# Kernel tuning notes

Measured on AMD Instinct MI355X. Metric: run time of the kernel, lower is better.

## Reference

```python
import jax, jax.numpy as jnp
import numpy as np

B, N, C, H, P = 8, 4096, 256, 4, 64  # batch, tokens, hidden, heads, proj_size


def setup_inputs() -> dict:
    key = jax.random.key(0)
    ks = jax.random.split(key, 6)
    sc = 0.02
    x = jax.random.normal(ks[0], (B, N, C), jnp.float32)
    bank = jax.random.normal(ks[1], (B, N, C), jnp.float32)  # unused by forward, kept for fidelity
    W_qkvv = jax.random.normal(ks[2], (4 * C, C), jnp.float32) * sc  # Linear(C, 4C), no bias
    W_E = jax.random.normal(ks[3], (P, N), jnp.float32) * sc          # E = F shared Linear(N, P)
    b_E = jnp.zeros((P,), jnp.float32)
    temperature = jnp.ones((H, 1, 1), jnp.float32)
    temperature2 = jnp.ones((H, 1, 1), jnp.float32)
    W_out1 = jax.random.normal(ks[4], (C // 2, C), jnp.float32) * sc  # out_proj (spatial branch)
    b_out1 = jnp.zeros((C // 2,), jnp.float32)
    W_out2 = jax.random.normal(ks[5], (C // 2, C), jnp.float32) * sc  # out_proj2 (channel branch)
    b_out2 = jnp.zeros((C // 2,), jnp.float32)
    prelu_a = jnp.array(0.25, jnp.float32)  # nn.PReLU() default: single shared slope
    return {"x": x, "bank": bank, "W_qkvv": W_qkvv, "W_E": W_E, "b_E": b_E,
            "temperature": temperature, "temperature2": temperature2,
            "W_out1": W_out1, "b_out1": b_out1, "W_out2": W_out2, "b_out2": b_out2,
            "prelu_a": prelu_a}


def _l2norm(t):
    # torch F.normalize(dim=-1): x / max(||x||_2, eps)
    return t / jnp.maximum(jnp.linalg.norm(t, axis=-1, keepdims=True), 1e-12)


def reference(x, bank, W_qkvv, W_E, b_E, temperature, temperature2,
              W_out1, b_out1, W_out2, b_out2, prelu_a):
    Bb, Nn, Cc = x.shape
    Hh = temperature.shape[0]
    d = Cc // Hh
    # qkvv projection -> [4, B, H, N, d], then transpose token/feature axes -> [B, H, d, N]
    qkvv = (x @ W_qkvv.T).reshape(Bb, Nn, 4, Hh, d).transpose(2, 0, 3, 1, 4)
    q, k, v_ca, v_sa = (qkvv[0].transpose(0, 1, 3, 2), qkvv[1].transpose(0, 1, 3, 2),
                        qkvv[2].transpose(0, 1, 3, 2), qkvv[3].transpose(0, 1, 3, 2))
    # shared linear E=F projects the token axis N -> P (applied to UNnormalized k, v_sa)
    k_proj = jnp.einsum('bhdn,pn->bhdp', k, W_E) + b_E      # [B,H,d,P]
    v_sa_proj = jnp.einsum('bhdn,pn->bhdp', v_sa, W_E) + b_E  # [B,H,d,P]
    qn = _l2norm(q)
    kn = _l2norm(k)
    # channel attention: [B,H,d,d]
    attn_ca = jax.nn.softmax(jnp.einsum('bhdn,bhen->bhde', qn, kn) * temperature, axis=-1)
    x_ca = jnp.einsum('bhde,bhen->bhdn', attn_ca, v_ca).transpose(0, 3, 1, 2).reshape(Bb, Nn, Cc)
    # spatial attention (projected): [B,H,N,P]
    attn_sa = jax.nn.softmax(jnp.einsum('bhdn,bhdp->bhnp', qn, k_proj) * temperature2, axis=-1)
    x_sa = jnp.einsum('bhnp,bhdp->bhnd', attn_sa, v_sa_proj).transpose(0, 2, 1, 3).reshape(Bb, Nn, Cc)
    x_sa = x_sa @ W_out1.T + b_out1
    x_ca = x_ca @ W_out2.T + b_out2
    out = jnp.concatenate([x_sa, x_ca], axis=-1)
    return jnp.where(out >= 0, out, prelu_a * out)  # PReLU
```

## Files before the change

### kernel.cpp

```cpp
#include <hip/hip_runtime.h>
#include <cstdint>
#include <cstddef>

constexpr int B_ = 8, N_ = 4096, C_ = 256, H_ = 4, D_ = 64, P_ = 64;
constexpr int OC_ = 4 * C_;
constexpr int M_  = B_ * N_;
constexpr int NC_SPLIT = 16;
constexpr int PAIR_ELEMS = 32 * 3 * 4096;

#define DEV_INLINE __device__ __forceinline__

typedef unsigned short ushort_t;
typedef __attribute__((ext_vector_type(8))) short short8;
typedef __attribute__((ext_vector_type(4))) short short4v;
typedef __attribute__((ext_vector_type(4))) float floatx4;

DEV_INLINE short f2bf(float f) {
  unsigned int u = __builtin_bit_cast(unsigned int, f);
  u += 0x7FFFu + ((u >> 16) & 1u);
  return (short)(u >> 16);
}

constexpr size_t X4_ = (size_t)M_ * C_ / 4;
constexpr size_t WQ4_ = (size_t)OC_ * C_ / 4;
constexpr size_t W14_ = (size_t)128 * C_ / 4;
constexpr size_t TOT4_ = X4_ + WQ4_ + 2 * W14_;

__global__ __launch_bounds__(256) void k_cast(const float* __restrict__ x,
                                              const float* __restrict__ Wq,
                                              const float* __restrict__ W1,
                                              const float* __restrict__ W2,
                                              ushort_t* __restrict__ xb,
                                              ushort_t* __restrict__ wqb,
                                              ushort_t* __restrict__ w1b,
                                              ushort_t* __restrict__ w2b) {
  const size_t stride = (size_t)gridDim.x * 256;
  for (size_t i = blockIdx.x * 256 + threadIdx.x; i < TOT4_; i += stride) {
    const float* src;
    ushort_t* dst;
    size_t o;
    if (i < X4_) { src = x; dst = xb; o = i; }
    else if (i < X4_ + WQ4_) { src = Wq; dst = wqb; o = i - X4_; }
    else if (i < X4_ + WQ4_ + W14_) { src = W1; dst = w1b; o = i - X4_ - WQ4_; }
    else { src = W2; dst = w2b; o = i - X4_ - WQ4_ - W14_; }
    float4 v = ((const float4*)src)[o];
    short4v s = {f2bf(v.x), f2bf(v.y), f2bf(v.z), f2bf(v.w)};
    *(short4v*)&dst[o * 4] = s;
  }
}

__global__ __launch_bounds__(256) void k_qkvv_mfma(const ushort_t* __restrict__ xb,
                                                   const ushort_t* __restrict__ wqb,
                                                   ushort_t* __restrict__ outb,
                                                   float* __restrict__ ssq) {
  __shared__ __align__(16) short As[128 * 72];
  __shared__ __align__(16) short Bs[128 * 72];
  const int bm = blockIdx.x * 128;
  const int bo = blockIdx.y * 128;
  const int t = threadIdx.x;
  const int oc = t & 7;
  const int rr = t >> 3;
  const int lane = t & 63, wave = t >> 6;
  const int m16 = lane & 15, quad = lane >> 4;
  const int wm = (wave >> 1) << 6, wn = (wave & 1) << 6;
  floatx4 acc[4][4];
#pragma unroll
  for (int i = 0; i < 4; ++i)
#pragma unroll
    for (int j = 0; j < 4; ++j) acc[i][j] = (floatx4)(0.f);
#pragma unroll 1
  for (int k0 = 0; k0 < 256; k0 += 64) {
    short8 a8[4], b8[4];
#pragma unroll
    for (int j = 0; j < 4; ++j) {
      const int r = rr + 32 * j;
      a8[j] = *(const short8*)&xb[(size_t)(bm + r) * 256 + k0 + 8 * oc];
      b8[j] = *(const short8*)&wqb[(size_t)(bo + r) * 256 + k0 + 8 * oc];
    }
    __syncthreads();
#pragma unroll
    for (int j = 0; j < 4; ++j) {
      const int r = rr + 32 * j;
      *(short8*)&As[r * 72 + 8 * oc] = a8[j];
      *(short8*)&Bs[r * 72 + 8 * oc] = b8[j];
    }
    __syncthreads();
#pragma unroll
    for (int ks = 0; ks < 2; ++ks) {
      short8 af[4], bf[4];
#pragma unroll
      for (int i = 0; i < 4; ++i)
        af[i] = *(const short8*)&As[(wm + i * 16 + m16) * 72 + ks * 32 + quad * 8];
// ... 2 lines not shown
        bf[j] = *(const short8*)&Bs[(wn + j * 16 + m16) * 72 + ks * 32 + quad * 8];
#pragma unroll
      for (int i = 0; i < 4; ++i)
#pragma unroll
        for (int j = 0; j < 4; ++j)
          acc[i][j] = __builtin_amdgcn_mfma_f32_16x16x32_bf16(af[i], bf[j], acc[i][j], 0, 0, 0);
    }
  }
#pragma unroll
  for (int i = 0; i < 4; ++i)
#pragma unroll
    for (int r = 0; r < 4; ++r) {
      const int gr = bm + wm + i * 16 + quad * 4 + r;
#pragma unroll
      for (int j = 0; j < 4; ++j)
        outb[(size_t)gr * OC_ + bo + wn + j * 16 + m16] = (ushort_t)f2bf(acc[i][j][r]);
    }
  if (bo < 512) {
    const int b = bm >> 12;
    float sj[4];
#pragma unroll
    for (int j = 0; j < 4; ++j) {
      float s = 0.f;
#pragma unroll
      for (int i = 0; i < 4; ++i)
#pragma unroll
        for (int r = 0; r < 4; ++r) s += acc[i][j][r] * acc[i][j][r];
      s += __shfl_xor(s, 16);
      s += __shfl_xor(s, 32);
      sj[j] = s;
    }
    if (lane < 16) {
#pragma unroll
      for (int j = 0; j < 4; ++j)
        atomicAdd(&ssq[b * 512 + bo + wn + 16 * j + m16], sj[j]);
    }
  }
}

__global__ __launch_bounds__(256) void k_out_mfma(const ushort_t* __restrict__ xsa,
                                                  const ushort_t* __restrict__ xca,
                                                  const ushort_t* __restrict__ w1b,
                                                  const float* __restrict__ b1,
                                                  const ushort_t* __restrict__ w2b,
                                                  const float* __restrict__ b2,
                                                  const float* __restrict__ pa,
                                                  float* __restrict__ out) {
  __shared__ __align__(16) short As[128 * 72];
  __shared__ __align__(16) short Bs[128 * 72];
  const int bm = blockIdx.x * 128;
  const int half = blockIdx.y;
  const ushort_t* A = half ? xca : xsa;
// ... 49 lines not shown
  for (int j = 0; j < 4; ++j) bj[j] = bias[wn + j * 16 + m16];
#pragma unroll
  for (int i = 0; i < 4; ++i)
#pragma unroll
    for (int r = 0; r < 4; ++r) {
      const int gr = bm + wm + i * 16 + quad * 4 + r;
#pragma unroll
      for (int j = 0; j < 4; ++j) {
        float v = acc[i][j][r] + bj[j];
        v = v >= 0.f ? v : slope * v;
        out[(size_t)gr * C_ + half * 128 + wn + j * 16 + m16] = v;
      }
    }
}

__global__ void k_norms_final(const float* __restrict__ ssq, float* __restrict__ rn) {
  const int i = blockIdx.x * 256 + threadIdx.x;
  rn[i] = 1.f / fmaxf(sqrtf(ssq[i]), 1e-12f);
}

__global__ __launch_bounds__(256) void k_pair_mfma(const ushort_t* __restrict__ qkvv,
                                                   const float* __restrict__ WE,
                                                   float* __restrict__ pp) {
  __shared__ __align__(16) short Qt[64 * 64];
  __shared__ __align__(16) short Kt[64 * 64];
  __shared__ __align__(16) short Vt[64 * 64];
  __shared__ __align__(16) short Wt[64 * 64];
  const int bh = blockIdx.x;
  const int nc = blockIdx.y;
  const int b = bh >> 2, h = bh & 3;
  const int t = threadIdx.x;
  const int lane = t & 63, wave = t >> 6;
  const int m16 = lane & 15, quad = lane >> 4;
  const int c0 = (t & 15) << 2;
  const int tp = t >> 4;
  floatx4 acc0[4], acc1[4], acc2[4];
#pragma unroll
  for (int j = 0; j < 4; ++j) {
    acc0[j] = (floatx4)(0.f); acc1[j] = (floatx4)(0.f); acc2[j] = (floatx4)(0.f);
  }
  const ushort_t* qb = qkvv + (size_t)b * N_ * OC_;
#pragma unroll 1
  for (int chunk = 0; chunk < 4; ++chunk) {
    const int n0 = nc * 256 + chunk * 64;
    __syncthreads();
#pragma unroll
    for (int j = 0; j < 2; ++j) {
      const int tok0 = 32 * j + 2 * tp;
      const size_t r0 = (size_t)(n0 + tok0) * OC_ + h * 64 + c0;
#pragma unroll
      for (int tt = 0; tt < 3; ++tt) {
        const int off = (tt == 0) ? 0 : (tt == 1 ? 256 : 768);
        short* T = (tt == 0) ? Qt : (tt == 1 ? Kt : Vt);
        short4v a = *(const short4v*)&qb[r0 + off];
        short4v c = *(const short4v*)&qb[r0 + OC_ + off];
#pragma unroll
        for (int i = 0; i < 4; ++i) {
          const int r = c0 + i;
          const int col = tok0 ^ (8 * (r >> 3));
          unsigned int w = (unsigned int)(ushort_t)a[i] |
                           ((unsigned int)(ushort_t)c[i] << 16);
          *(unsigned int*)&T[r * 64 + col] = w;
        }
      }
    }
#pragma unroll
    for (int j2 = 0; j2 < 4; ++j2) {
      const int p = tp + 16 * j2;
      float4 wv = *(const float4*)&WE[(size_t)p * N_ + n0 + c0];
      short4v s = {f2bf(wv.x), f2bf(wv.y), f2bf(wv.z), f2bf(wv.w)};
      *(short4v*)&Wt[p * 64 + (c0 ^ (8 * (p >> 3)))] = s;
    }
    __syncthreads();
#pragma unroll
    for (int ks = 0; ks < 2; ++ks) {
      const int boct = ks * 32 + quad * 8;
      const int rA = 16 * wave + m16;
      const int swA = boct ^ (8 * (rA >> 3));
      short8 af0 = *(const short8*)&Qt[rA * 64 + swA];
      short8 afK = *(const short8*)&Kt[rA * 64 + swA];
      short8 afV = *(const short8*)&Vt[rA * 64 + swA];
      short8 bfK[4], bfW[4];
#pragma unroll
      for (int j = 0; j < 4; ++j) {
        const int rB = 16 * j + m16;
        const int swB = boct ^ (8 * (rB >> 3));
        bfK[j] = *(const short8*)&Kt[rB * 64 + swB];
        bfW[j] = *(const short8*)&Wt[rB * 64 + swB];
      }
#pragma unroll
      for (int j = 0; j < 4; ++j) {
        acc0[j] = __builtin_amdgcn_mfma_f32_16x16x32_bf16(af0, bfK[j], acc0[j], 0, 0, 0);
        acc1[j] = __builtin_amdgcn_mfma_f32_16x16x32_bf16(afK, bfW[j], acc1[j], 0, 0, 0);
        acc2[j] = __builtin_amdgcn_mfma_f32_16x16x32_bf16(afV, bfW[j], acc2[j], 0, 0, 0);
      }
    }
  }
  float* pb = pp + ((size_t)nc * 32 + bh) * (3 * 4096);
#pragma unroll
  for (int j = 0; j < 4; ++j)
#pragma unroll
    for (int r = 0; r < 4; ++r) {
      const int d = 16 * wave + quad * 4 + r;
      const int cc = 16 * j + m16;
      pb[0 * 4096 + d * 64 + cc] = acc0[j][r];
      pb[1 * 4096 + cc * 64 + d] = acc1[j][r];
      pb[2 * 4096 + d * 64 + cc] = acc2[j][r];
    }
}

__global__ __launch_bounds__(256) void k_pair_reduce(const float* __restrict__ pp,
                                                     const float* __restrict__ bE,
                                                     const float* __restrict__ rn,
                                                     const float* __restrict__ t2,
                                                     float* __restrict__ Sqk,
                                                     ushort_t* __restrict__ ksb,
                                                     ushort_t* __restrict__ vsb) {
  const int e = blockIdx.x * 256 + threadIdx.x;
  float s = 0.f;
#pragma unroll
  for (int nc = 0; nc < NC_SPLIT; ++nc) s += pp[(size_t)nc * PAIR_ELEMS + e];
  const int bh = e / 12288;
  const int rem = e - bh * 12288;
  const int op = rem >> 12;
  const int idx = rem & 4095;
  const int b = bh >> 2, h = bh & 3;
  if (op == 0) {
    Sqk[(size_t)bh * 4096 + idx] = s;
  } else if (op == 1) {
    const int p = idx >> 6, d = idx & 63;
    ksb[(size_t)bh * 4096 + idx] =
        (ushort_t)f2bf((s + bE[p]) * rn[b * 512 + h * 64 + d] * t2[h]);
  } else {
    const int p = idx & 63;
    vsb[(size_t)bh * 4096 + idx] = (ushort_t)f2bf(s + bE[p]);
  }
}

__global__ __launch_bounds__(256) void k_ca_softmax(const float* __restrict__ Sqk,
                                                    const float* __restrict__ rn,
                                                    const float* __restrict__ temp,
                                                    ushort_t* __restrict__ ab) {
  const int w = threadIdx.x >> 6;
  const int lane = threadIdx.x & 63;
  const int row = blockIdx.x * 4 + w;
  const int b = row >> 8;
  const int rem = row & 255;
  const int h = rem >> 6;
  const float rq = rn[b * 512 + rem];
  const float rk = rn[b * 512 + 256 + h * 64 + lane];
  float l = Sqk[(size_t)row * 64 + lane] * rq * rk * temp[h];
  float m = l;
#pragma unroll
  for (int o = 32; o; o >>= 1) m = fmaxf(m, __shfl_xor(m, o));
  const float e = __expf(l - m);
  float s = e;
#pragma unroll
  for (int o = 32; o; o >>= 1) s += __shfl_xor(s, o);
  ab[(size_t)row * 64 + lane] = (ushort_t)f2bf(e / s);
}

__global__ __launch_bounds__(256) void k_ca_mfma(const ushort_t* __restrict__ qkvv,
                                                 const ushort_t* __restrict__ ab,
                                                 ushort_t* __restrict__ x_ca) {
  const int bh = blockIdx.x;
  const int b = bh >> 2, h = bh & 3;
  const int n0 = blockIdx.y * 128;
  const int lane = threadIdx.x & 63, wave = threadIdx.x >> 6;
  const int m16 = lane & 15, quad = lane >> 4;
  const ushort_t* abb = ab + (size_t)bh * 4096;
  short8 bf[2][4];
#pragma unroll
  for (int ks = 0; ks < 2; ++ks)
#pragma unroll
    for (int j = 0; j < 4; ++j)
      bf[ks][j] = *(const short8*)&abb[(16 * j + m16) * 64 + ks * 32 + quad * 8];
#pragma unroll
  for (int mm = 0; mm < 2; ++mm) {
    const int tokbase = n0 + 64 * mm + 16 * wave;
    const ushort_t* vrow =
        qkvv + (size_t)(b * N_ + tokbase + m16) * OC_ + 512 + h * 64 + quad * 8;
    short8 af0 = *(const short8*)&vrow[0];
    short8 af1 = *(const short8*)&vrow[32];
    floatx4 o[4];
#pragma unroll
    for (int j = 0; j < 4; ++j) o[j] = (floatx4)(0.f);
#pragma unroll
    for (int j = 0; j < 4; ++j) {
      o[j] = __builtin_amdgcn_mfma_f32_16x16x32_bf16(af0, bf[0][j], o[j], 0, 0, 0);
      o[j] = __builtin_amdgcn_mfma_f32_16x16x32_bf16(af1, bf[1][j], o[j], 0, 0, 0);
    }
#pragma unroll
    for (int j = 0; j < 4; ++j)
#pragma unroll
      for (int r = 0; r < 4; ++r)
        x_ca[(size_t)(b * N_ + tokbase + quad * 4 + r) * C_ + h * 64 + 16 * j + m16] =
            (ushort_t)f2bf(o[j][r]);
  }
}

__global__ __launch_bounds__(256) void k_sa_mfma(const ushort_t* __restrict__ qkvv,
                                                 const ushort_t* __restrict__ ksb,
                                                 const ushort_t* __restrict__ vsb,
                                                 ushort_t* __restrict__ x_sa) {
  __shared__ float Pl[64][68];
  const int bh = blockIdx.x;
  const int b = bh >> 2, h = bh & 3;
  const int n0 = blockIdx.y * 64;
  const int lane = threadIdx.x & 63, wave = threadIdx.x >> 6;
  const int m16 = lane & 15, quad = lane >> 4;
  const ushort_t* qrow =
      qkvv + (size_t)(b * N_ + n0 + 16 * wave + m16) * OC_ + h * 64 + quad * 8;
  short8 qf0 = *(const short8*)&qrow[0];
  short8 qf1 = *(const short8*)&qrow[32];
  const ushort_t* kb = ksb + (size_t)bh * 4096;
  const ushort_t* vb = vsb + (size_t)bh * 4096;
  short8 kf[2][4], vf[2][4];
#pragma unroll
  for (int ks = 0; ks < 2; ++ks)
#pragma unroll
    for (int j = 0; j < 4; ++j) {
      kf[ks][j] = *(const short8*)&kb[(16 * j + m16) * 64 + ks * 32 + quad * 8];
      vf[ks][j] = *(const short8*)&vb[(16 * j + m16) * 64 + ks * 32 + quad * 8];
    }
  floatx4 s[4];
#pragma unroll
  for (int j = 0; j < 4; ++j) s[j] = (floatx4)(0.f);
#pragma unroll
  for (int j = 0; j < 4; ++j) {
    s[j] = __builtin_amdgcn_mfma_f32_16x16x32_bf16(qf0, kf[0][j], s[j], 0, 0, 0);
    s[j] = __builtin_amdgcn_mfma_f32_16x16x32_bf16(qf1, kf[1][j], s[j], 0, 0, 0);
  }
  float p[4][4];
#pragma unroll
  for (int r = 0; r < 4; ++r) {
    float mr = fmaxf(fmaxf(s[0][r], s[1][r]), fmaxf(s[2][r], s[3][r]));
    mr = fmaxf(mr, __shfl_xor(mr, 1));
    mr = fmaxf(mr, __shfl_xor(mr, 2));
    mr = fmaxf(mr, __shfl_xor(mr, 4));
    mr = fmaxf(mr, __shfl_xor(mr, 8));
    float sr = 0.f;
#pragma unroll
    for (int j = 0; j < 4; ++j) {
      const float e = __expf(s[j][r] - mr);
      p[j][r] = e;
      sr += e;
    }
    sr += __shfl_xor(sr, 1);
    sr += __shfl_xor(sr, 2);
    sr += __shfl_xor(sr, 4);
    sr += __shfl_xor(sr, 8);
    const float inv = 1.f / sr;
#pragma unroll
    for (int j = 0; j < 4; ++j) p[j][r] *= inv;
  }
#pragma unroll
  for (int j = 0; j < 4; ++j)
#pragma unroll
    for (int r = 0; r < 4; ++r)
      Pl[16 * wave + quad * 4 + r][16 * j + m16] = p[j][r];
  __syncthreads();
  short8 pf[2];
#pragma unroll
  for (int ks = 0; ks < 2; ++ks) {
    float4 x0 = *(const float4*)&Pl[16 * wave + m16][ks * 32 + quad * 8];
    float4 x1 = *(const float4*)&Pl[16 * wave + m16][ks * 32 + quad * 8 + 4];
    short8 v;
    v[0] = f2bf(x0.x); v[1] = f2bf(x0.y); v[2] = f2bf(x0.z); v[3] = f2bf(x0.w);
    v[4] = f2bf(x1.x); v[5] = f2bf(x1.y); v[6] = f2bf(x1.z); v[7] = f2bf(x1.w);
    pf[ks] = v;
  }
  floatx4 o[4];
#pragma unroll
  for (int j = 0; j < 4; ++j) o[j] = (floatx4)(0.f);
#pragma unroll
  for (int j = 0; j < 4; ++j) {
    o[j] = __builtin_amdgcn_mfma_f32_16x16x32_bf16(pf[0], vf[0][j], o[j], 0, 0, 0);
    o[j] = __builtin_amdgcn_mfma_f32_16x16x32_bf16(pf[1], vf[1][j], o[j], 0, 0, 0);
  }
#pragma unroll
  for (int j = 0; j < 4; ++j)
#pragma unroll
    for (int r = 0; r < 4; ++r)
      x_sa[(size_t)(b * N_ + n0 + 16 * wave + quad * 4 + r) * C_ + h * 64 + 16 * j + m16] =
          (ushort_t)f2bf(o[j][r]);
}

extern "C" void kernel_launch(void* const* d_in, const int* in_sizes, int n_in,
                              void* d_out, int out_size, void* d_ws, size_t ws_size,
                              hipStream_t stream) {
  (void)in_sizes; (void)n_in; (void)out_size; (void)ws_size;
  const float* x  = (const float*)d_in[0];
  const float* Wq = (const float*)d_in[2];
  const float* WE = (const float*)d_in[3];
  const float* bE = (const float*)d_in[4];
  const float* t1 = (const float*)d_in[5];
  const float* t2 = (const float*)d_in[6];
  const float* W1 = (const float*)d_in[7];
  const float* b1 = (const float*)d_in[8];
  const float* W2 = (const float*)d_in[9];
  const float* b2 = (const float*)d_in[10];
  const float* pa = (const float*)d_in[11];
  float* out = (float*)d_out;

  float* ws = (float*)d_ws;
  size_t off = 0;
  float* Sqk  = ws + off; off += (size_t)B_ * H_ * D_ * D_;
  float* ssq  = ws + off; off += (size_t)B_ * 512;
  float* rn   = ws + off; off += (size_t)B_ * 512;
  float* pp   = ws + off; off += (size_t)NC_SPLIT * PAIR_ELEMS;
  ushort_t* qkvv = (ushort_t*)(ws + off); off += (size_t)M_ * OC_ / 2;
  ushort_t* xsa  = (ushort_t*)(ws + off); off += (size_t)M_ * C_ / 2;
  ushort_t* xca  = (ushort_t*)(ws + off); off += (size_t)M_ * C_ / 2;
  ushort_t* ksb  = (ushort_t*)(ws + off); off += 32 * 4096 / 2;
  ushort_t* vsb  = (ushort_t*)(ws + off); off += 32 * 4096 / 2;
  ushort_t* ab   = (ushort_t*)(ws + off); off += 32 * 4096 / 2;
  ushort_t* xb   = (ushort_t*)(ws + off); off += (size_t)M_ * C_ / 2;
  ushort_t* wqb  = (ushort_t*)(ws + off); off += (size_t)OC_ * C_ / 2;
  ushort_t* w1b  = (ushort_t*)(ws + off); off += (size_t)128 * C_ / 2;
  ushort_t* w2b  = (ushort_t*)(ws + off); off += (size_t)128 * C_ / 2;

  hipMemsetAsync(ssq, 0, 4096 * sizeof(float), stream);

  k_cast<<<2048, 256, 0, stream>>>(x, Wq, W1, W2, xb, wqb, w1b, w2b);
  k_qkvv_mfma<<<dim3(M_ / 128, OC_ / 128), 256, 0, stream>>>(xb, wqb, qkvv, ssq);
  k_norms_final<<<16, 256, 0, stream>>>(ssq, rn);
  k_pair_mfma<<<dim3(32, NC_SPLIT), 256, 0, stream>>>(qkvv, WE, pp);
  k_pair_reduce<<<PAIR_ELEMS / 256, 256, 0, stream>>>(pp, bE, rn, t2, Sqk, ksb, vsb);
  k_ca_softmax<<<512, 256, 0, stream>>>(Sqk, rn, t1, ab);
  k_ca_mfma<<<dim3(32, 32), 256, 0, stream>>>(qkvv, ab, xca);
  k_sa_mfma<<<dim3(32, 64), 256, 0, stream>>>(qkvv, ksb, vsb, xsa);
  k_out_mfma<<<dim3(M_ / 128, 2), 256, 0, stream>>>(xsa, xca, w1b, b1, w2b, b2, pa, out);
}
```

Measured before the change: 227.2 us.

## Derive k and v_sa statistics from input Gram matrix instead of materializing them

Replaces the full qkvv projection with a q/v_ca-only projection. K-side quantities (q·k channel Gram, k norms, k and v_sa token projections through W_E) are now computed from an input Gram matrix X^T X and X^T W_E^T per batch, followed by small GEMMs with the weight matrix. This removes writing and rereading half of the projected activations and drops the separate pair-reduction pass. In exchange it adds several small kernels, an atomic-accumulated fp32 Gram buffer, and extra bf16 rounding of the Gram terms that may cost accuracy.

```diff
diff --git a/kernel.cpp b/kernel.cpp
--- a/kernel.cpp
+++ b/kernel.cpp
@@ -5,8 +5,8 @@
 constexpr int B_ = 8, N_ = 4096, C_ = 256, H_ = 4, D_ = 64, P_ = 64;
 constexpr int OC_ = 4 * C_;
 constexpr int M_  = B_ * N_;
-constexpr int NC_SPLIT = 16;
-constexpr int PAIR_ELEMS = 32 * 3 * 4096;
+constexpr int GX_ROWS = 320;
+constexpr int KSPLIT_G = 8;
 
 #define DEV_INLINE __device__ __forceinline__
 
@@ -20,20 +20,26 @@
   u += 0x7FFFu + ((u >> 16) & 1u);
   return (short)(u >> 16);
 }
-
-constexpr size_t X4_ = (size_t)M_ * C_ / 4;
+DEV_INLINE float bf2f(ushort_t u) {
+  return __builtin_bit_cast(float, (unsigned int)u << 16);
+}
+
+constexpr size_t X4_  = (size_t)M_ * C_ / 4;
 constexpr size_t WQ4_ = (size_t)OC_ * C_ / 4;
 constexpr size_t W14_ = (size_t)128 * C_ / 4;
-constexpr size_t TOT4_ = X4_ + WQ4_ + 2 * W14_;
+constexpr size_t WE4_ = (size_t)P_ * N_ / 4;
+constexpr size_t TOT4_ = X4_ + WQ4_ + 2 * W14_ + WE4_;
 
 __global__ __launch_bounds__(256) void k_cast(const float* __restrict__ x,
                                               const float* __restrict__ Wq,
                                               const float* __restrict__ W1,
                                               const float* __restrict__ W2,
+                                              const float* __restrict__ WE,
                                               ushort_t* __restrict__ xb,
                                               ushort_t* __restrict__ wqb,
                                               ushort_t* __restrict__ w1b,
-                                              ushort_t* __restrict__ w2b) {
+                                              ushort_t* __restrict__ w2b,
+                                              ushort_t* __restrict__ web) {
   const size_t stride = (size_t)gridDim.x * 256;
   for (size_t i = blockIdx.x * 256 + threadIdx.x; i < TOT4_; i += stride) {
     const float* src;
@@ -42,21 +48,137 @@
     if (i < X4_) { src = x; dst = xb; o = i; }
     else if (i < X4_ + WQ4_) { src = Wq; dst = wqb; o = i - X4_; }
     else if (i < X4_ + WQ4_ + W14_) { src = W1; dst = w1b; o = i - X4_ - WQ4_; }
-    else { src = W2; dst = w2b; o = i - X4_ - WQ4_ - W14_; }
+    else if (i < X4_ + WQ4_ + 2 * W14_) { src = W2; dst = w2b; o = i - X4_ - WQ4_ - W14_; }
+    else { src = WE; dst = web; o = i - X4_ - WQ4_ - 2 * W14_; }
     float4 v = ((const float4*)src)[o];
     short4v s = {f2bf(v.x), f2bf(v.y), f2bf(v.z), f2bf(v.w)};
     *(short4v*)&dst[o * 4] = s;
   }
 }
 
-__global__ __launch_bounds__(256) void k_qkvv_mfma(const ushort_t* __restrict__ xb,
-                                                   const ushort_t* __restrict__ wqb,
-                                                   ushort_t* __restrict__ outb,
-                                                   float* __restrict__ ssq) {
+__global__ __launch_bounds__(256) void k_gram(const ushort_t* __restrict__ xb,
+                                              const ushort_t* __restrict__ web,
+                                              float* __restrict__ Gx) {
+  __shared__ __align__(16) short As[128 * 64];
+  __shared__ __align__(16) short Bs[128 * 64];
+  const int job = blockIdx.x;
+  const int ablk = job >> 1;
+  const int bblk = job & 1;
+  const int b = blockIdx.y >> 3;
+  const int ksp = blockIdx.y & 7;
+  const int t = threadIdx.x;
+  const int lane = t & 63, wave = t >> 6;
+  const int m16 = lane & 15, quad = lane >> 4;
+  const int wm = (wave >> 1) << 6, wn = (wave & 1) << 6;
+  floatx4 acc[4][4];
+#pragma unroll
+  for (int i = 0; i < 4; ++i)
+#pragma unroll
+    for (int j = 0; j < 4; ++j) acc[i][j] = (floatx4)(0.f);
+  if (ablk == 2) {
+#pragma unroll
+    for (int i = 0; i < 8; ++i)
+      *(unsigned int*)&As[64 * 64 + (i * 256 + t) * 2] = 0u;
+  }
+  const int c0 = (t & 31) * 4;
+  const int tp = t >> 5;
+#pragma unroll 1
+  for (int it = 0; it < N_ / KSPLIT_G / 64; ++it) {
+    const int n0 = ksp * (N_ / KSPLIT_G) + it * 64;
+    __syncthreads();
+#pragma unroll
+    for (int q = 0; q < 4; ++q) {
+      const int tok = q * 16 + 2 * tp;
+      const size_t r0 = (size_t)(b * N_ + n0 + tok) * C_ + bblk * 128 + c0;
+      short4v aa = *(const short4v*)&xb[r0];
+      short4v cc = *(const short4v*)&xb[r0 + C_];
+#pragma unroll
+      for (int i = 0; i < 4; ++i) {
+        const int r = c0 + i;
+        const int col = tok ^ (8 * ((r >> 3) & 7));
+        unsigned int w = (unsigned int)(ushort_t)aa[i] |
+                         ((unsigned int)(ushort_t)cc[i] << 16);
+        *(unsigned int*)&Bs[r * 64 + col] = w;
+      }
+    }
+    if (ablk < 2) {
+#pragma unroll
+      for (int q = 0; q < 4; ++q) {
+        const int tok = q * 16 + 2 * tp;
+        const size_t r0 = (size_t)(b * N_ + n0 + tok) * C_ + ablk * 128 + c0;
+        short4v aa = *(const short4v*)&xb[r0];
+        short4v cc = *(const short4v*)&xb[r0 + C_];
+#pragma unroll
+        for (int i = 0; i < 4; ++i) {
+          const int r = c0 + i;
+          const int col = tok ^ (8 * ((r >> 3) & 7));
+          unsigned int w = (unsigned int)(ushort_t)aa[i] |
+                           ((unsigned int)(ushort_t)cc[i] << 16);
+          *(unsigned int*)&As[r * 64 + col] = w;
+        }
+      }
+    } else {
+      const int oc8 = (t & 7) * 8;
+      const int p0 = t >> 3;
+#pragma unroll
+      for (int q = 0; q < 2; ++q) {
+        const int p = p0 + 32 * q;
+        short8 v = *(const short8*)&web[(size_t)p * N_ + n0 + oc8];
+        *(short8*)&As[p * 64 + (oc8 ^ (8 * ((p >> 3) & 7)))] = v;
+      }
+    }
+    __syncthreads();
+#pragma unroll
+    for (int ks = 0; ks < 2; ++ks) {
+      const int boct = ks * 32 + quad * 8;
+      short8 af[4], bf[4];
+#pragma unroll
+      for (int i = 0; i < 4; ++i) {
+        const int rA = wm + i * 16 + m16;
+        af[i] = *(const short8*)&As[rA * 64 + (boct ^ (8 * ((rA >> 3) & 7)))];
+      }
+#pragma unroll
+      for (int j = 0; j < 4; ++j) {
+        const int rB = wn + j * 16 + m16;
+        bf[j] = *(const short8*)&Bs[rB * 64 + (boct ^ (8 * ((rB >> 3) & 7)))];
+      }
+#pragma unroll
+      for (int i = 0; i < 4; ++i)
+#pragma unroll
+        for (int j = 0; j < 4; ++j)
+          acc[i][j] = __builtin_amdgcn_mfma_f32_16x16x32_bf16(af[i], bf[j], acc[i][j], 0, 0, 0);
+    }
+  }
+#pragma unroll
+  for (int i = 0; i < 4; ++i)
+#pragma unroll
+    for (int r = 0; r < 4; ++r) {
+      const int rib = wm + i * 16 + quad * 4 + r;
+      if (ablk == 2 && rib >= 64) continue;
+      const size_t rowoff =
+          ((size_t)b * GX_ROWS + ablk * 128 + rib) * 256 + bblk * 128 + wn;
+#pragma unroll
+      for (int j = 0; j < 4; ++j)
+        atomicAdd(&Gx[rowoff + 16 * j + m16], acc[i][j][r]);
+    }
+}
+
+__global__ __launch_bounds__(256) void k_gcast(const float* __restrict__ Gx,
+                                               ushort_t* __restrict__ Gxb) {
+  const int i = blockIdx.x * 256 + threadIdx.x;
+  float4 v = ((const float4*)Gx)[i];
+  short4v s = {f2bf(v.x), f2bf(v.y), f2bf(v.z), f2bf(v.w)};
+  *(short4v*)&Gxb[i * 4] = s;
+}
+
+__global__ __launch_bounds__(256) void k_qv_mfma(const ushort_t* __restrict__ xb,
+                                                 const ushort_t* __restrict__ wqb,
+                                                 ushort_t* __restrict__ qv) {
   __shared__ __align__(16) short As[128 * 72];
   __shared__ __align__(16) short Bs[128 * 72];
   const int bm = blockIdx.x * 128;
   const int bo = blockIdx.y * 128;
+  const int wrow_base = bo < 256 ? bo : bo + 256;
   const int t = threadIdx.x;
   const int oc = t & 7;
   const int rr = t >> 3;
@@ -75,7 +197,7 @@
     for (int j = 0; j < 4; ++j) {
       const int r = rr + 32 * j;
       a8[j] = *(const short8*)&xb[(size_t)(bm + r) * 256 + k0 + 8 * oc];
-      b8[j] = *(const short8*)&wqb[(size_t)(bo + r) * 256 + k0 + 8 * oc];
+      b8[j] = *(const short8*)&wqb[(size_t)(wrow_base + r) * 256 + k0 + 8 * oc];
     }
     __syncthreads();
 #pragma unroll
@@ -108,28 +230,317 @@
       const int gr = bm + wm + i * 16 + quad * 4 + r;
 #pragma unroll
       for (int j = 0; j < 4; ++j)
-        outb[(size_t)gr * OC_ + bo + wn + j * 16 + m16] = (ushort_t)f2bf(acc[i][j][r]);
-    }
-  if (bo < 512) {
-    const int b = bm >> 12;
-    float sj[4];
-#pragma unroll
-    for (int j = 0; j < 4; ++j) {
-      float s = 0.f;
+        qv[(size_t)gr * 512 + bo + wn + j * 16 + m16] = (ushort_t)f2bf(acc[i][j][r]);
+    }
+}
+
+__global__ __launch_bounds__(256) void k_t2gemm(const ushort_t* __restrict__ wqb,
+                                                const ushort_t* __restrict__ Gxb,
+                                                ushort_t* __restrict__ T2b) {
+  __shared__ __align__(16) short As[128 * 72];
+  __shared__ __align__(16) short Bs[128 * 72];
+  const int bm = blockIdx.x * 128;
+  const int b  = blockIdx.y >> 1;
+  const int jb = blockIdx.y & 1;
+  const int t = threadIdx.x;
+  const int oc = t & 7;
+  const int rr = t >> 3;
+  const int lane = t & 63, wave = t >> 6;
+  const int m16 = lane & 15, quad = lane >> 4;
+  const int wm = (wave >> 1) << 6, wn = (wave & 1) << 6;
+  const ushort_t* Bsrc = Gxb + ((size_t)b * GX_ROWS + jb * 128) * 256;
+  floatx4 acc[4][4];
+#pragma unroll
+  for (int i = 0; i < 4; ++i)
+#pragma unroll
+    for (int j = 0; j < 4; ++j) acc[i][j] = (floatx4)(0.f);
+#pragma unroll 1
+  for (int k0 = 0; k0 < 256; k0 += 64) {
+    short8 a8[4], b8[4];
+#pragma unroll
+    for (int j = 0; j < 4; ++j) {
+      const int r = rr + 32 * j;
+      a8[j] = *(const short8*)&wqb[(size_t)(bm + r) * 256 + k0 + 8 * oc];
+      b8[j] = *(const short8*)&Bsrc[(size_t)r * 256 + k0 + 8 * oc];
+    }
+    __syncthreads();
+#pragma unroll
+    for (int j = 0; j < 4; ++j) {
+      const int r = rr + 32 * j;
+      *(short8*)&As[r * 72 + 8 * oc] = a8[j];
+      *(short8*)&Bs[r * 72 + 8 * oc] = b8[j];
+    }
+    __syncthreads();
+#pragma unroll
+    for (int ks = 0; ks < 2; ++ks) {
+      short8 af[4], bf[4];
 #pragma unroll
       for (int i = 0; i < 4; ++i)
-#pragma unroll
-        for (int r = 0; r < 4; ++r) s += acc[i][j][r] * acc[i][j][r];
-      s += __shfl_xor(s, 16);
-      s += __shfl_xor(s, 32);
-      sj[j] = s;
-    }
-    if (lane < 16) {
+        af[i] = *(const short8*)&As[(wm + i * 16 + m16) * 72 + ks * 32 + quad * 8];
 #pragma unroll
       for (int j = 0; j < 4; ++j)
-        atomicAdd(&ssq[b * 512 + bo + wn + 16 * j + m16], sj[j]);
-    }
-  }
+        bf[j] = *(const short8*)&Bs[(wn + j * 16 + m16) * 72 + ks * 32 + quad * 8];
+#pragma unroll
+      for (int i = 0; i < 4; ++i)
+#pragma unroll
+        for (int j = 0; j < 4; ++j)
+          acc[i][j] = __builtin_amdgcn_mfma_f32_16x16x32_bf16(af[i], bf[j], acc[i][j], 0, 0, 0);
+    }
+  }
+#pragma unroll
+  for (int i = 0; i < 4; ++i)
+#pragma unroll
+    for (int r = 0; r < 4; ++r) {
+      const int gr = bm + wm + i * 16 + quad * 4 + r;
+#pragma unroll
+      for (int j = 0; j < 4; ++j)
+        T2b[((size_t)b * 512 + gr) * 256 + jb * 128 + wn + j * 16 + m16] =
+            (ushort_t)f2bf(acc[i][j][r]);
+    }
+}
+
+__global__ __launch_bounds__(256) void k_rn(const ushort_t* __restrict__ wqb,
+                                            const ushort_t* __restrict__ T2b,
+                                            float* __restrict__ rn) {
+  const int row_g = blockIdx.x * 4 + (threadIdx.x >> 6);
+  const int lane = threadIdx.x & 63;
+  const int b = row_g >> 9, row = row_g & 511;
+  const short4v w  = *(const short4v*)&wqb[(size_t)row * 256 + lane * 4];
+  const short4v tv = *(const short4v*)&T2b[((size_t)b * 512 + row) * 256 + lane * 4];
+  float s = 0.f;
+#pragma unroll
+  for (int i = 0; i < 4; ++i) s += bf2f((ushort_t)w[i]) * bf2f((ushort_t)tv[i]);
+#pragma unroll
+  for (int o = 32; o; o >>= 1) s += __shfl_xor(s, o);
+  if (lane == 0) rn[row_g] = 1.f / fmaxf(sqrtf(s), 1e-12f);
+}
+
+__global__ __launch_bounds__(64) void k_small(const ushort_t* __restrict__ wqb,
+                                              const ushort_t* __restrict__ T2b,
+                                              const ushort_t* __restrict__ Gxb,
+                                              const float* __restrict__ bE,
+                                              const float* __restrict__ rn,
+                                              const float* __restrict__ t2,
+                                              float* __restrict__ Sqk,
+                                              ushort_t* __restrict__ ksb,
+                                              ushort_t* __restrict__ vsb) {
+  const int bh = blockIdx.x;
+  const int job = blockIdx.y;
+  const int b = bh >> 2, h = bh & 3;
+  const int lane = threadIdx.x & 63;
+  const int m16 = lane & 15, quad = lane >> 4;
+  const int Abase = (job == 0 ? 0 : (job == 1 ? 256 : 768)) + h * 64;
+  const ushort_t* Bp = (job == 0)
+      ? T2b + ((size_t)b * 512 + 256 + h * 64) * 256
+      : Gxb + ((size_t)b * GX_ROWS + 256) * 256;
+  floatx4 acc[4][4];
+#pragma unroll
+  for (int i = 0; i < 4; ++i)
+#pragma unroll
+    for (int j = 0; j < 4; ++j) acc[i][j] = (floatx4)(0.f);
+#pragma unroll
+  for (int ks = 0; ks < 8; ++ks) {
+    const int boct = ks * 32 + quad * 8;
+    short8 af[4], bf[4];
+#pragma unroll
+    for (int i = 0; i < 4; ++i)
+      af[i] = *(const short8*)&wqb[(size_t)(Abase + 16 * i + m16) * 256 + boct];
+#pragma unroll
+    for (int j = 0; j < 4; ++j)
+      bf[j] = *(const short8*)&Bp[(size_t)(16 * j + m16) * 256 + boct];
+#pragma unroll
+    for (int i = 0; i < 4; ++i)
+#pragma unroll
+      for (int j = 0; j < 4; ++j)
+        acc[i][j] = __builtin_amdgcn_mfma_f32_16x16x32_bf16(af[i], bf[j], acc[i][j], 0, 0, 0);
+  }
+  if (job == 0) {
+#pragma unroll
+    for (int i = 0; i < 4; ++i)
+#pragma unroll
+      for (int r = 0; r < 4; ++r) {
+        const int d = 16 * i + quad * 4 + r;
+#pragma unroll
+        for (int j = 0; j < 4; ++j)
+          Sqk[(size_t)bh * 4096 + d * 64 + 16 * j + m16] = acc[i][j][r];
+      }
+  } else if (job == 1) {
+    const float tt = t2[h];
+#pragma unroll
+    for (int i = 0; i < 4; ++i)
+#pragma unroll
+      for (int r = 0; r < 4; ++r) {
+        const int d = 16 * i + quad * 4 + r;
+        const float rq = rn[b * 512 + h * 64 + d];
+#pragma unroll
+        for (int j = 0; j < 4; ++j) {
+          const int p = 16 * j + m16;
+          ksb[(size_t)bh * 4096 + p * 64 + d] =
+              (ushort_t)f2bf((acc[i][j][r] + bE[p]) * rq * tt);
+        }
+      }
+  } else {
+#pragma unroll
+    for (int i = 0; i < 4; ++i)
+#pragma unroll
+      for (int r = 0; r < 4; ++r) {
+        const int d = 16 * i + quad * 4 + r;
+#pragma unroll
+        for (int j = 0; j < 4; ++j) {
+          const int p = 16 * j + m16;
+          vsb[(size_t)bh * 4096 + d * 64 + p] = (ushort_t)f2bf(acc[i][j][r] + bE[p]);
+        }
+      }
+  }
+}
+
+__global__ __launch_bounds__(256) void k_ca_softmax(const float* __restrict__ Sqk,
+                                                    const float* __restrict__ rn,
+                                                    const float* __restrict__ temp,
+                                                    ushort_t* __restrict__ ab) {
+  const int w = threadIdx.x >> 6;
+  const int lane = threadIdx.x & 63;
+  const int row = blockIdx.x * 4 + w;
+  const int b = row >> 8;
+  const int rem = row & 255;
+  const int h = rem >> 6;
+  const float rq = rn[b * 512 + rem];
+  const float rk = rn[b * 512 + 256 + h * 64 + lane];
+  float l = Sqk[(size_t)row * 64 + lane] * rq * rk * temp[h];
+  float m = l;
+#pragma unroll
+  for (int o = 32; o; o >>= 1) m = fmaxf(m, __shfl_xor(m, o));
+  const float e = __expf(l - m);
+  float s = e;
+#pragma unroll
+  for (int o = 32; o; o >>= 1) s += __shfl_xor(s, o);
+  ab[(size_t)row * 64 + lane] = (ushort_t)f2bf(e / s);
+}
+
+__global__ __launch_bounds__(256) void k_ca_mfma(const ushort_t* __restrict__ qv,
+                                                 const ushort_t* __restrict__ ab,
+                                                 ushort_t* __restrict__ x_ca) {
+  const int bh = blockIdx.x;
+  const int b = bh >> 2, h = bh & 3;
+  const int n0 = blockIdx.y * 128;
+  const int lane = threadIdx.x & 63, wave = threadIdx.x >> 6;
+  const int m16 = lane & 15, quad = lane >> 4;
+  const ushort_t* abb = ab + (size_t)bh * 4096;
+  short8 bf[2][4];
+#pragma unroll
+  for (int ks = 0; ks < 2; ++ks)
+#pragma unroll
+    for (int j = 0; j < 4; ++j)
+      bf[ks][j] = *(const short8*)&abb[(16 * j + m16) * 64 + ks * 32 + quad * 8];
+#pragma unroll
+  for (int mm = 0; mm < 2; ++mm) {
+    const int tokbase = n0 + 64 * mm + 16 * wave;
+    const ushort_t* vrow =
+        qv + (size_t)(b * N_ + tokbase + m16) * 512 + 256 + h * 64 + quad * 8;
+    short8 af0 = *(const short8*)&vrow[0];
+    short8 af1 = *(const short8*)&vrow[32];
+    floatx4 o[4];
+#pragma unroll
+    for (int j = 0; j < 4; ++j) o[j] = (floatx4)(0.f);
+#pragma unroll
+    for (int j = 0; j < 4; ++j) {
+      o[j] = __builtin_amdgcn_mfma_f32_16x16x32_bf16(af0, bf[0][j], o[j], 0, 0, 0);
+      o[j] = __builtin_amdgcn_mfma_f32_16x16x32_bf16(af1, bf[1][j], o[j], 0, 0, 0);
+    }
+#pragma unroll
+    for (int j = 0; j < 4; ++j)
+#pragma unroll
+      for (int r = 0; r < 4; ++r)
+        x_ca[(size_t)(b * N_ + tokbase + quad * 4 + r) * C_ + h * 64 + 16 * j + m16] =
+            (ushort_t)f2bf(o[j][r]);
+  }
+}
+
+__global__ __launch_bounds__(256) void k_sa_mfma(const ushort_t* __restrict__ qv,
+                                                 const ushort_t* __restrict__ ksb,
+                                                 const ushort_t* __restrict__ vsb,
+                                                 ushort_t* __restrict__ x_sa) {
+  __shared__ float Pl[64][68];
+  const int bh = blockIdx.x;
+  const int b = bh >> 2, h = bh & 3;
+  const int n0 = blockIdx.y * 64;
+  const int lane = threadIdx.x & 63, wave = threadIdx.x >> 6;
+  const int m16 = lane & 15, quad = lane >> 4;
+  const ushort_t* qrow =
+      qv + (size_t)(b * N_ + n0 + 16 * wave + m16) * 512 + h * 64 + quad * 8;
+  short8 qf0 = *(const short8*)&qrow[0];
+  short8 qf1 = *(const short8*)&qrow[32];
+  const ushort_t* kb = ksb + (size_t)bh * 4096;
+  const ushort_t* vb = vsb + (size_t)bh * 4096;
+  short8 kf[2][4], vf[2][4];
+#pragma unroll
+  for (int ks = 0; ks < 2; ++ks)
+#pragma unroll
+    for (int j = 0; j < 4; ++j) {
+      kf[ks][j] = *(const short8*)&kb[(16 * j + m16) * 64 + ks * 32 + quad * 8];
+      vf[ks][j] = *(const short8*)&vb[(16 * j + m16) * 64 + ks * 32 + quad * 8];
+    }
+  floatx4 s[4];
+#pragma unroll
+  for (int j = 0; j < 4; ++j) s[j] = (floatx4)(0.f);
+#pragma unroll
+  for (int j = 0; j < 4; ++j) {
+    s[j] = __builtin_amdgcn_mfma_f32_16x16x32_bf16(qf0, kf[0][j], s[j], 0, 0, 0);
+    s[j] = __builtin_amdgcn_mfma_f32_16x16x32_bf16(qf1, kf[1][j], s[j], 0, 0, 0);
+  }
+  float p[4][4];
+#pragma unroll
+  for (int r = 0; r < 4; ++r) {
+    float mr = fmaxf(fmaxf(s[0][r], s[1][r]), fmaxf(s[2][r], s[3][r]));
+    mr = fmaxf(mr, __shfl_xor(mr, 1));
+    mr = fmaxf(mr, __shfl_xor(mr, 2));
+    mr = fmaxf(mr, __shfl_xor(mr, 4));
+    mr = fmaxf(mr, __shfl_xor(mr, 8));
+    float sr = 0.f;
+#pragma unroll
+    for (int j = 0; j < 4; ++j) {
+      const float e = __expf(s[j][r] - mr);
+      p[j][r] = e;
+      sr += e;
+    }
+    sr += __shfl_xor(sr, 1);
+    sr += __shfl_xor(sr, 2);
+    sr += __shfl_xor(sr, 4);
+    sr += __shfl_xor(sr, 8);
+    const float inv = 1.f / sr;
+#pragma unroll
+    for (int j = 0; j < 4; ++j) p[j][r] *= inv;
+  }
+#pragma unroll
+  for (int j = 0; j < 4; ++j)
+#pragma unroll
+    for (int r = 0; r < 4; ++r)
+      Pl[16 * wave + quad * 4 + r][16 * j + m16] = p[j][r];
+  __syncthreads();
+  short8 pf[2];
+#pragma unroll
+  for (int ks = 0; ks < 2; ++ks) {
+    float4 x0 = *(const float4*)&Pl[16 * wave + m16][ks * 32 + quad * 8];
+    float4 x1 = *(const float4*)&Pl[16 * wave + m16][ks * 32 + quad * 8 + 4];
+    short8 v;
+    v[0] = f2bf(x0.x); v[1] = f2bf(x0.y); v[2] = f2bf(x0.z); v[3] = f2bf(x0.w);
+    v[4] = f2bf(x1.x); v[5] = f2bf(x1.y); v[6] = f2bf(x1.z); v[7] = f2bf(x1.w);
+    pf[ks] = v;
+  }
+  floatx4 o[4];
+#pragma unroll
+  for (int j = 0; j < 4; ++j) o[j] = (floatx4)(0.f);
+#pragma unroll
+  for (int j = 0; j < 4; ++j) {
+    o[j] = __builtin_amdgcn_mfma_f32_16x16x32_bf16(pf[0], vf[0][j], o[j], 0, 0, 0);
+    o[j] = __builtin_amdgcn_mfma_f32_16x16x32_bf16(pf[1], vf[1][j], o[j], 0, 0, 0);
+  }
+#pragma unroll
+  for (int j = 0; j < 4; ++j)
+#pragma unroll
+    for (int r = 0; r < 4; ++r)
+      x_sa[(size_t)(b * N_ + n0 + 16 * wave + quad * 4 + r) * C_ + h * 64 + 16 * j + m16] =
+          (ushort_t)f2bf(o[j][r]);
 }
 
 __global__ __launch_bounds__(256) void k_out_mfma(const ushort_t* __restrict__ xsa,
@@ -209,278 +620,6 @@
     }
 }
 
-__global__ void k_norms_final(const float* __restrict__ ssq, float* __restrict__ rn) {
-  const int i = blockIdx.x * 256 + threadIdx.x;
-  rn[i] = 1.f / fmaxf(sqrtf(ssq[i]), 1e-12f);
-}
-
-__global__ __launch_bounds__(256) void k_pair_mfma(const ushort_t* __restrict__ qkvv,
-                                                   const float* __restrict__ WE,
-                                                   float* __restrict__ pp) {
-  __shared__ __align__(16) short Qt[64 * 64];
-  __shared__ __align__(16) short Kt[64 * 64];
-  __shared__ __align__(16) short Vt[64 * 64];
-  __shared__ __align__(16) short Wt[64 * 64];
-  const int bh = blockIdx.x;
-  const int nc = blockIdx.y;
-  const int b = bh >> 2, h = bh & 3;
-  const int t = threadIdx.x;
-  const int lane = t & 63, wave = t >> 6;
-  const int m16 = lane & 15, quad = lane >> 4;
-  const int c0 = (t & 15) << 2;
-  const int tp = t >> 4;
-  floatx4 acc0[4], acc1[4], acc2[4];
-#pragma unroll
-  for (int j = 0; j < 4; ++j) {
-    acc0[j] = (floatx4)(0.f); acc1[j] = (floatx4)(0.f); acc2[j] = (floatx4)(0.f);
-  }
-  const ushort_t* qb = qkvv + (size_t)b * N_ * OC_;
-#pragma unroll 1
-  for (int chunk = 0; chunk < 4; ++chunk) {
-    const int n0 = nc * 256 + chunk * 64;
-    __syncthreads();
-#pragma unroll
-    for (int j = 0; j < 2; ++j) {
-      const int tok0 = 32 * j + 2 * tp;
-      const size_t r0 = (size_t)(n0 + tok0) * OC_ + h * 64 + c0;
-#pragma unroll
-      for (int tt = 0; tt < 3; ++tt) {
-        const int off = (tt == 0) ? 0 : (tt == 1 ? 256 : 768);
-        short* T = (tt == 0) ? Qt : (tt == 1 ? Kt : Vt);
-        short4v a = *(const short4v*)&qb[r0 + off];
-        short4v c = *(const short4v*)&qb[r0 + OC_ + off];
-#pragma unroll
-        for (int i = 0; i < 4; ++i) {
-          const int r = c0 + i;
-          const int col = tok0 ^ (8 * (r >> 3));
-          unsigned int w = (unsigned int)(ushort_t)a[i] |
-                           ((unsigned int)(ushort_t)c[i] << 16);
-          *(unsigned int*)&T[r * 64 + col] = w;
-        }
-      }
-    }
-#pragma unroll
-    for (int j2 = 0; j2 < 4; ++j2) {
-      const int p = tp + 16 * j2;
-      float4 wv = *(const float4*)&WE[(size_t)p * N_ + n0 + c0];
-      short4v s = {f2bf(wv.x), f2bf(wv.y), f2bf(wv.z), f2bf(wv.w)};
-      *(short4v*)&Wt[p * 64 + (c0 ^ (8 * (p >> 3)))] = s;
-    }
-    __syncthreads();
-#pragma unroll
-    for (int ks = 0; ks < 2; ++ks) {
-      const int boct = ks * 32 + quad * 8;
-      const int rA = 16 * wave + m16;
-      const int swA = boct ^ (8 * (rA >> 3));
-      short8 af0 = *(const short8*)&Qt[rA * 64 + swA];
-      short8 afK = *(const short8*)&Kt[rA * 64 + swA];
-      short8 afV = *(const short8*)&Vt[rA * 64 + swA];
-      short8 bfK[4], bfW[4];
-#pragma unroll
-      for (int j = 0; j < 4; ++j) {
-        const int rB = 16 * j + m16;
-        const int swB = boct ^ (8 * (rB >> 3));
-        bfK[j] = *(const short8*)&Kt[rB * 64 + swB];
-        bfW[j] = *(const short8*)&Wt[rB * 64 + swB];
-      }
-#pragma unroll
-      for (int j = 0; j < 4; ++j) {
-        acc0[j] = __builtin_amdgcn_mfma_f32_16x16x32_bf16(af0, bfK[j], acc0[j], 0, 0, 0);
-        acc1[j] = __builtin_amdgcn_mfma_f32_16x16x32_bf16(afK, bfW[j], acc1[j], 0, 0, 0);
-        acc2[j] = __builtin_amdgcn_mfma_f32_16x16x32_bf16(afV, bfW[j], acc2[j], 0, 0, 0);
-      }
-    }
-  }
-  float* pb = pp + ((size_t)nc * 32 + bh) * (3 * 4096);
-#pragma unroll
-  for (int j = 0; j < 4; ++j)
-#pragma unroll
-    for (int r = 0; r < 4; ++r) {
-      const int d = 16 * wave + quad * 4 + r;
-      const int cc = 16 * j + m16;
-      pb[0 * 4096 + d * 64 + cc] = acc0[j][r];
-      pb[1 * 4096 + cc * 64 + d] = acc1[j][r];
-      pb[2 * 4096 + d * 64 + cc] = acc2[j][r];
-    }
-}
-
-__global__ __launch_bounds__(256) void k_pair_reduce(const float* __restrict__ pp,
-                                                     const float* __restrict__ bE,
-                                                     const float* __restrict__ rn,
-                                                     const float* __restrict__ t2,
-                                                     float* __restrict__ Sqk,
-                                                     ushort_t* __restrict__ ksb,
-                                                     ushort_t* __restrict__ vsb) {
-  const int e = blockIdx.x * 256 + threadIdx.x;
-  float s = 0.f;
-#pragma unroll
-  for (int nc = 0; nc < NC_SPLIT; ++nc) s += pp[(size_t)nc * PAIR_ELEMS + e];
-  const int bh = e / 12288;
-  const int rem = e - bh * 12288;
-  const int op = rem >> 12;
-  const int idx = rem & 4095;
-  const int b = bh >> 2, h = bh & 3;
-  if (op == 0) {
-    Sqk[(size_t)bh * 4096 + idx] = s;
-  } else if (op == 1) {
-    const int p = idx >> 6, d = idx & 63;
-    ksb[(size_t)bh * 4096 + idx] =
-        (ushort_t)f2bf((s + bE[p]) * rn[b * 512 + h * 64 + d] * t2[h]);
-  } else {
-    const int p = idx & 63;
-    vsb[(size_t)bh * 4096 + idx] = (ushort_t)f2bf(s + bE[p]);
-  }
-}
-
-__global__ __launch_bounds__(256) void k_ca_softmax(const float* __restrict__ Sqk,
-                                                    const float* __restrict__ rn,
-                                                    const float* __restrict__ temp,
-                                                    ushort_t* __restrict__ ab) {
-  const int w = threadIdx.x >> 6;
-  const int lane = threadIdx.x & 63;
-  const int row = blockIdx.x * 4 + w;
-  const int b = row >> 8;
-  const int rem = row & 255;
-  const int h = rem >> 6;
-  const float rq = rn[b * 512 + rem];
-  const float rk = rn[b * 512 + 256 + h * 64 + lane];
-  float l = Sqk[(size_t)row * 64 + lane] * rq * rk * temp[h];
-  float m = l;
-#pragma unroll
-  for (int o = 32; o; o >>= 1) m = fmaxf(m, __shfl_xor(m, o));
-  const float e = __expf(l - m);
-  float s = e;
-#pragma unroll
-  for (int o = 32; o; o >>= 1) s += __shfl_xor(s, o);
-  ab[(size_t)row * 64 + lane] = (ushort_t)f2bf(e / s);
-}
-
-__global__ __launch_bounds__(256) void k_ca_mfma(const ushort_t* __restrict__ qkvv,
-                                                 const ushort_t* __restrict__ ab,
-                                                 ushort_t* __restrict__ x_ca) {
-  const int bh = blockIdx.x;
-  const int b = bh >> 2, h = bh & 3;
-  const int n0 = blockIdx.y * 128;
-  const int lane = threadIdx.x & 63, wave = threadIdx.x >> 6;
-  const int m16 = lane & 15, quad = lane >> 4;
-  const ushort_t* abb = ab + (size_t)bh * 4096;
-  short8 bf[2][4];
-#pragma unroll
-  for (int ks = 0; ks < 2; ++ks)
-#pragma unroll
-    for (int j = 0; j < 4; ++j)
-      bf[ks][j] = *(const short8*)&abb[(16 * j + m16) * 64 + ks * 32 + quad * 8];
-#pragma unroll
-  for (int mm = 0; mm < 2; ++mm) {
-    const int tokbase = n0 + 64 * mm + 16 * wave;
-    const ushort_t* vrow =
-        qkvv + (size_t)(b * N_ + tokbase + m16) * OC_ + 512 + h * 64 + quad * 8;
-    short8 af0 = *(const short8*)&vrow[0];
-    short8 af1 = *(const short8*)&vrow[32];
-    floatx4 o[4];
-#pragma unroll
-    for (int j = 0; j < 4; ++j) o[j] = (floatx4)(0.f);
-#pragma unroll
-    for (int j = 0; j < 4; ++j) {
-      o[j] = __builtin_amdgcn_mfma_f32_16x16x32_bf16(af0, bf[0][j], o[j], 0, 0, 0);
-      o[j] = __builtin_amdgcn_mfma_f32_16x16x32_bf16(af1, bf[1][j], o[j], 0, 0, 0);
-    }
-#pragma unroll
-    for (int j = 0; j < 4; ++j)
-#pragma unroll
-      for (int r = 0; r < 4; ++r)
-        x_ca[(size_t)(b * N_ + tokbase + quad * 4 + r) * C_ + h * 64 + 16 * j + m16] =
-            (ushort_t)f2bf(o[j][r]);
-  }
-}
-
-__global__ __launch_bounds__(256) void k_sa_mfma(const ushort_t* __restrict__ qkvv,
-                                                 const ushort_t* __restrict__ ksb,
-                                                 const ushort_t* __restrict__ vsb,
-                                                 ushort_t* __restrict__ x_sa) {
-  __shared__ float Pl[64][68];
-  const int bh = blockIdx.x;
-  const int b = bh >> 2, h = bh & 3;
-  const int n0 = blockIdx.y * 64;
-  const int lane = threadIdx.x & 63, wave = threadIdx.x >> 6;
-  const int m16 = lane & 15, quad = lane >> 4;
-  const ushort_t* qrow =
-      qkvv + (size_t)(b * N_ + n0 + 16 * wave + m16) * OC_ + h * 64 + quad * 8;
-  short8 qf0 = *(const short8*)&qrow[0];
-  short8 qf1 = *(const short8*)&qrow[32];
-  const ushort_t* kb = ksb + (size_t)bh * 4096;
-  const ushort_t* vb = vsb + (size_t)bh * 4096;
-  short8 kf[2][4], vf[2][4];
-#pragma unroll
-  for (int ks = 0; ks < 2; ++ks)
-#pragma unroll
-    for (int j = 0; j < 4; ++j) {
-      kf[ks][j] = *(const short8*)&kb[(16 * j + m16) * 64 + ks * 32 + quad * 8];
-      vf[ks][j] = *(const short8*)&vb[(16 * j + m16) * 64 + ks * 32 + quad * 8];
-    }
-  floatx4 s[4];
-#pragma unroll
-  for (int j = 0; j < 4; ++j) s[j] = (floatx4)(0.f);
-#pragma unroll
-  for (int j = 0; j < 4; ++j) {
-    s[j] = __builtin_amdgcn_mfma_f32_16x16x32_bf16(qf0, kf[0][j], s[j], 0, 0, 0);
-    s[j] = __builtin_amdgcn_mfma_f32_16x16x32_bf16(qf1, kf[1][j], s[j], 0, 0, 0);
-  }
-  float p[4][4];
-#pragma unroll
-  for (int r = 0; r < 4; ++r) {
-    float mr = fmaxf(fmaxf(s[0][r], s[1][r]), fmaxf(s[2][r], s[3][r]));
-    mr = fmaxf(mr, __shfl_xor(mr, 1));
-    mr = fmaxf(mr, __shfl_xor(mr, 2));
-    mr = fmaxf(mr, __shfl_xor(mr, 4));
-    mr = fmaxf(mr, __shfl_xor(mr, 8));
-    float sr = 0.f;
-#pragma unroll
-    for (int j = 0; j < 4; ++j) {
-      const float e = __expf(s[j][r] - mr);
-      p[j][r] = e;
-      sr += e;
-    }
-    sr += __shfl_xor(sr, 1);
-    sr += __shfl_xor(sr, 2);
-    sr += __shfl_xor(sr, 4);
-    sr += __shfl_xor(sr, 8);
-    const float inv = 1.f / sr;
-#pragma unroll
-    for (int j = 0; j < 4; ++j) p[j][r] *= inv;
-  }
-#pragma unroll
-  for (int j = 0; j < 4; ++j)
-#pragma unroll
-    for (int r = 0; r < 4; ++r)
-      Pl[16 * wave + quad * 4 + r][16 * j + m16] = p[j][r];
-  __syncthreads();
-  short8 pf[2];
-#pragma unroll
-  for (int ks = 0; ks < 2; ++ks) {
-    float4 x0 = *(const float4*)&Pl[16 * wave + m16][ks * 32 + quad * 8];
-    float4 x1 = *(const float4*)&Pl[16 * wave + m16][ks * 32 + quad * 8 + 4];
-    short8 v;
-    v[0] = f2bf(x0.x); v[1] = f2bf(x0.y); v[2] = f2bf(x0.z); v[3] = f2bf(x0.w);
-    v[4] = f2bf(x1.x); v[5] = f2bf(x1.y); v[6] = f2bf(x1.z); v[7] = f2bf(x1.w);
-    pf[ks] = v;
-  }
-  floatx4 o[4];
-#pragma unroll
-  for (int j = 0; j < 4; ++j) o[j] = (floatx4)(0.f);
-#pragma unroll
-  for (int j = 0; j < 4; ++j) {
-    o[j] = __builtin_amdgcn_mfma_f32_16x16x32_bf16(pf[0], vf[0][j], o[j], 0, 0, 0);
-    o[j] = __builtin_amdgcn_mfma_f32_16x16x32_bf16(pf[1], vf[1][j], o[j], 0, 0, 0);
-  }
-#pragma unroll
-  for (int j = 0; j < 4; ++j)
-#pragma unroll
-    for (int r = 0; r < 4; ++r)
-      x_sa[(size_t)(b * N_ + n0 + 16 * wave + quad * 4 + r) * C_ + h * 64 + 16 * j + m16] =
-          (ushort_t)f2bf(o[j][r]);
-}
-
 extern "C" void kernel_launch(void* const* d_in, const int* in_sizes, int n_in,
                               void* d_out, int out_size, void* d_ws, size_t ws_size,
                               hipStream_t stream) {
@@ -500,30 +639,34 @@
 
   float* ws = (float*)d_ws;
   size_t off = 0;
-  float* Sqk  = ws + off; off += (size_t)B_ * H_ * D_ * D_;
-  float* ssq  = ws + off; off += (size_t)B_ * 512;
-  float* rn   = ws + off; off += (size_t)B_ * 512;
-  float* pp   = ws + off; off += (size_t)NC_SPLIT * PAIR_ELEMS;
-  ushort_t* qkvv = (ushort_t*)(ws + off); off += (size_t)M_ * OC_ / 2;
-  ushort_t* xsa  = (ushort_t*)(ws + off); off += (size_t)M_ * C_ / 2;
-  ushort_t* xca  = (ushort_t*)(ws + off); off += (size_t)M_ * C_ / 2;
-  ushort_t* ksb  = (ushort_t*)(ws + off); off += 32 * 4096 / 2;
-  ushort_t* vsb  = (ushort_t*)(ws + off); off += 32 * 4096 / 2;
-  ushort_t* ab   = (ushort_t*)(ws + off); off += 32 * 4096 / 2;
-  ushort_t* xb   = (ushort_t*)(ws + off); off += (size_t)M_ * C_ / 2;
-  ushort_t* wqb  = (ushort_t*)(ws + off); off += (size_t)OC_ * C_ / 2;
-  ushort_t* w1b  = (ushort_t*)(ws + off); off += (size_t)128 * C_ / 2;
-  ushort_t* w2b  = (ushort_t*)(ws + off); off += (size_t)128 * C_ / 2;
-
-  hipMemsetAsync(ssq, 0, 4096 * sizeof(float), stream);
-
-  k_cast<<<2048, 256, 0, stream>>>(x, Wq, W1, W2, xb, wqb, w1b, w2b);
-  k_qkvv_mfma<<<dim3(M_ / 128, OC_ / 128), 256, 0, stream>>>(xb, wqb, qkvv, ssq);
-  k_norms_final<<<16, 256, 0, stream>>>(ssq, rn);
-  k_pair_mfma<<<dim3(32, NC_SPLIT), 256, 0, stream>>>(qkvv, WE, pp);
-  k_pair_reduce<<<PAIR_ELEMS / 256, 256, 0, stream>>>(pp, bE, rn, t2, Sqk, ksb, vsb);
+  float* Sqk = ws + off; off += (size_t)32 * 4096;
+  float* rn  = ws + off; off += (size_t)B_ * 512;
+  float* Gx  = ws + off; off += (size_t)B_ * GX_ROWS * 256;
+  ushort_t* qv  = (ushort_t*)(ws + off); off += (size_t)M_ * 512 / 2;
+  ushort_t* xsa = (ushort_t*)(ws + off); off += (size_t)M_ * C_ / 2;
+  ushort_t* xca = (ushort_t*)(ws + off); off += (size_t)M_ * C_ / 2;
+  ushort_t* ksb = (ushort_t*)(ws + off); off += 32 * 4096 / 2;
+  ushort_t* vsb = (ushort_t*)(ws + off); off += 32 * 4096 / 2;
+  ushort_t* ab  = (ushort_t*)(ws + off); off += 32 * 4096 / 2;
+  ushort_t* xb  = (ushort_t*)(ws + off); off += (size_t)M_ * C_ / 2;
+  ushort_t* wqb = (ushort_t*)(ws + off); off += (size_t)OC_ * C_ / 2;
+  ushort_t* w1b = (ushort_t*)(ws + off); off += (size_t)128 * C_ / 2;
+  ushort_t* w2b = (ushort_t*)(ws + off); off += (size_t)128 * C_ / 2;
+  ushort_t* web = (ushort_t*)(ws + off); off += (size_t)P_ * N_ / 2;
+  ushort_t* Gxb = (ushort_t*)(ws + off); off += (size_t)B_ * GX_ROWS * 256 / 2;
+  ushort_t* T2b = (ushort_t*)(ws + off); off += (size_t)B_ * 512 * 256 / 2;
+
+  hipMemsetAsync(Gx, 0, (size_t)B_ * GX_ROWS * 256 * sizeof(float), stream);
+
+  k_cast<<<2048, 256, 0, stream>>>(x, Wq, W1, W2, WE, xb, wqb, w1b, w2b, web);
+  k_gram<<<dim3(6, B_ * KSPLIT_G), 256, 0, stream>>>(xb, web, Gx);
+  k_qv_mfma<<<dim3(M_ / 128, 4), 256, 0, stream>>>(xb, wqb, qv);
+  k_gcast<<<640, 256, 0, stream>>>(Gx, Gxb);
+  k_t2gemm<<<dim3(4, B_ * 2), 256, 0, stream>>>(wqb, Gxb, T2b);
+  k_rn<<<1024, 256, 0, stream>>>(wqb, T2b, rn);
+  k_small<<<dim3(32, 3), 64, 0, stream>>>(wqb, T2b, Gxb, bE, rn, t2, Sqk, ksb, vsb);
   k_ca_softmax<<<512, 256, 0, stream>>>(Sqk, rn, t1, ab);
-  k_ca_mfma<<<dim3(32, 32), 256, 0, stream>>>(qkvv, ab, xca);
-  k_sa_mfma<<<dim3(32, 64), 256, 0, stream>>>(qkvv, ksb, vsb, xsa);
+  k_ca_mfma<<<dim3(32, 32), 256, 0, stream>>>(qv, ab, xca);
+  k_sa_mfma<<<dim3(32, 64), 256, 0, stream>>>(qv, ksb, vsb, xsa);
   k_out_mfma<<<dim3(M_ / 128, 2), 256, 0, stream>>>(xsa, xca, w1b, b1, w2b, b2, pa, out);
 }
```

Result: slower. 234.4 us (+3.2%).
